# Performance work log

Hardware: AMD Instinct MI355X
Metric: run time of the kernel (lower is better)

The kernel has to match this reference:

```python
import jax, jax.numpy as jnp
import numpy as np

EPS = 1e-8
FS = 10000
WIN_LEN = 256          # N_FRAME
HOP = WIN_LEN // 2     # 128
NFFT = 2 * WIN_LEN     # 512
NUMBAND = 15
MINFREQ = 150
N_INTEL = 30           # N, number of frames per intelligibility segment
BETA = -15.0
DYN_RANGE = 40.0


def _thirdoct(fs, nfft, num_bands, min_freq):
    """One-third octave band matrix (pystoi.utils.thirdoct)."""
    f = np.linspace(0, fs, nfft + 1)[: nfft // 2 + 1]
    k = np.arange(num_bands, dtype=np.float64)
    freq_low = min_freq * np.power(2.0, (2 * k - 1) / 6)
    freq_high = min_freq * np.power(2.0, (2 * k + 1) / 6)
    obm = np.zeros((num_bands, len(f)), dtype=np.float32)
    for i in range(num_bands):
        fl = int(np.argmin(np.square(f - freq_low[i])))
        fh = int(np.argmin(np.square(f - freq_high[i])))
        obm[i, fl:fh] = 1.0
    return obm


def _frame(x, framelen, hop):
    """x: (B, T) -> (B, nf, framelen) sliding frames (static index gather)."""
    T = x.shape[-1]
    nf = (T - framelen) // hop + 1
    idx = np.arange(framelen)[None, :] + hop * np.arange(nf)[:, None]
    return x[:, idx]


def _stoi(est, tgt, win, obm):
    B = tgt.shape[0]
    # ---- VAD: remove silent frames (stable-partition kept frames to front) ----
    xf = _frame(tgt, WIN_LEN, HOP) * win           # (B, nf, L)
    yf = _frame(est, WIN_LEN, HOP) * win
    energies = 20.0 * jnp.log10(jnp.linalg.norm(xf, axis=-1) + EPS)  # (B, nf)
    mask = (energies.max(-1, keepdims=True) - DYN_RANGE - energies) < 0
    nf = xf.shape[1]
    # stable argsort: kept (mask=True -> key 0) frames first, original order preserved
    order = jnp.argsort(jnp.logical_not(mask).astype(jnp.int32), axis=-1)
    xf = jnp.take_along_axis(xf, order[..., None], axis=1)
    yf = jnp.take_along_axis(yf, order[..., None], axis=1)
    counts = mask.sum(-1)                          # (B,) number of kept frames
    keep = (jnp.arange(nf)[None, :] < counts[:, None]).astype(xf.dtype)
    xf = xf * keep[..., None]
    yf = yf * keep[..., None]

    # ---- overlap-and-add (framelen == 2 * hop) -> (B, (nf+1)*HOP) ----
    def ola(fr):
        a = fr[:, :, :HOP].reshape(B, -1)
        b = fr[:, :, HOP:].reshape(B, -1)
        return jnp.pad(a, ((0, 0), (0, HOP))) + jnp.pad(b, ((0, 0), (HOP, 0)))

    x_sil = ola(xf)
    y_sil = ola(yf)

    # mask sorted descending then first element dropped -> ones at positions < count-1
    m = (jnp.arange(nf - 1)[None, :] < (counts[:, None] - 1)).astype(xf.dtype)  # (B, nf-1)

    # ---- STFT via framing + rfft (last frame dropped, as in module) ----
    def stft(x):
        fr = _frame(x, WIN_LEN, HOP)[:, :-1] * win        # (B, nf-1, L)
        return jnp.fft.rfft(fr, n=NFFT, axis=-1)          # (B, nf-1, F)

    x_spec = stft(x_sil) * m[..., None]
    y_spec = stft(y_sil) * m[..., None]

    # ---- one-third octave band energies ----
    x_tob = jnp.sqrt(jnp.einsum('kf,bnf->bkn', obm, jnp.abs(x_spec) ** 2) + EPS)
    y_tob = jnp.sqrt(jnp.einsum('kf,bnf->bkn', obm, jnp.abs(y_spec) ** 2) + EPS)

    # ---- N_INTEL-frame segments (unfold) ----
    n_stft = x_tob.shape[-1]
    M = n_stft - N_INTEL + 1
    sidx = np.arange(N_INTEL)[:, None] + np.arange(M)[None, :]
    x_seg = x_tob[:, :, sidx]                      # (B, K, N, M)
    y_seg = y_tob[:, :, sidx]
    m2 = m[:, N_INTEL - 1:]                        # (B, M)
    x_seg = x_seg * m2[:, None, None, :]
    y_seg = y_seg * m2[:, None, None, :]

    # ---- clipped, normalized correlation (non-extended STOI) ----
    norm_const = jnp.linalg.norm(x_seg, axis=2, keepdims=True) / (
        jnp.linalg.norm(y_seg, axis=2, keepdims=True) + EPS)
    clip_val = 10.0 ** (-BETA / 20.0)
    y_prim = jnp.minimum(y_seg * norm_const, x_seg * (1.0 + clip_val))
    y_prim = y_prim - y_prim.mean(2, keepdims=True)
    x_c = x_seg - x_seg.mean(2, keepdims=True)
    y_prim = y_prim / (jnp.linalg.norm(y_prim, axis=2, keepdims=True) + EPS)
    x_c = x_c / (jnp.linalg.norm(x_c, axis=2, keepdims=True) + EPS)
    corr = (y_prim * x_c).sum(2).mean(1)           # (B, M)
    out = corr.sum(-1) / (m2.sum(-1) + EPS)        # (B,)
    return -out


def setup_inputs() -> dict:
    key = jax.random.key(0)
    k1, k2 = jax.random.split(key)
    B, T = 32, 320000
    targets = jax.random.normal(k1, (B, T), dtype=jnp.float32)
    est_targets = targets + 0.3 * jax.random.normal(k2, (B, T), dtype=jnp.float32)
    win = jnp.asarray(np.hanning(WIN_LEN + 2)[1:-1], dtype=jnp.float32)
    obm = jnp.asarray(_thirdoct(FS, NFFT, NUMBAND, MINFREQ))
    return {"est_targets": est_targets, "targets": targets, "win": win, "obm": obm}


def reference(est_targets, targets, win, obm):
    return _stoi(est_targets, targets, win, obm)
```

## Files before the change

### kernel.cpp

```cpp
#include <hip/hip_runtime.h>
#include <math.h>

#define EPSF 1e-8f
#define WIN_LEN 256
#define HOP 128
#define NBINS 257
#define NUMBAND 15
#define NFRAMES 2499
#define NSTFT 2498
#define N_INTEL 30
#define NSEG 2469
#define NB 32
#define T_LEN 320000
#define CLIP_VAL 5.623413251903491f
#define NHALF 2500
#define AB_STRIDE 2560

typedef float v2f __attribute__((ext_vector_type(2)));
typedef float v4f __attribute__((ext_vector_type(4)));

__device__ __forceinline__ void pk_fma_blo(v2f& d, v2f a, v2f b) {
    asm("v_pk_fma_f32 %0, %1, %2, %0 op_sel:[0,0,0] op_sel_hi:[1,0,1]"
        : "+v"(d) : "v"(a), "v"(b));
}
__device__ __forceinline__ void pk_fma_rot(v2f& d, v2f a, v2f b) {
    asm("v_pk_fma_f32 %0, %1, %2, %0 op_sel:[1,1,0] op_sel_hi:[0,1,1] neg_lo:[1,0,0]"
        : "+v"(d) : "v"(a), "v"(b));
}
__device__ __forceinline__ void pk_rot(v2f& cs, v2f cksk) {
    v2f t;
    asm("v_pk_mul_f32 %0, %1, %2 op_sel:[0,0] op_sel_hi:[1,0]"
        : "=v"(t) : "v"(cs), "v"(cksk));
    asm("v_pk_fma_f32 %0, %0, %1, %2 op_sel:[1,1,0] op_sel_hi:[0,1,1] neg_lo:[1,0,0]"
        : "+v"(cs) : "v"(cksk), "v"(t));
}
__device__ __forceinline__ v2f pk_cmul(v2f a, v2f b) {
    v2f t;
    asm("v_pk_mul_f32 %0, %1, %2 op_sel:[0,0] op_sel_hi:[1,0]"
        : "=v"(t) : "v"(a), "v"(b));
    asm("v_pk_fma_f32 %0, %1, %2, %0 op_sel:[1,1,0] op_sel_hi:[0,1,1] neg_lo:[1,0,0]"
        : "+v"(t) : "v"(a), "v"(b));
    return t;
}

#define WS_COUNTS   0
#define WS_BANDLO   512
#define WS_BANDHI   768
#define WS_ACC      1024
#define WS_SRCFRM   2048
#define WS_XTOB     324096
#define WS_YTOB     5120512

__global__ __launch_bounds__(256)
void k1a_ab(const float* __restrict__ tgt, const float* __restrict__ win,
            float2* __restrict__ ab)
{
    const int b = blockIdx.x;
    const int h = blockIdx.y * 256 + threadIdx.x;
    if (h >= NHALF) return;
    const float* xp = tgt + (size_t)b * T_LEN + (size_t)h * HOP;
    float sa = 0.f, sb = 0.f;
    #pragma unroll 4
    for (int u = 0; u < HOP; u += 4) {
        const float4 xv = *(const float4*)(xp + u);
        const float4 wl = *(const float4*)(win + u);
        const float4 wh = *(const float4*)(win + HOP + u);
        float a;
        a = xv.x * wl.x; sa = fmaf(a, a, sa);
        a = xv.y * wl.y; sa = fmaf(a, a, sa);
        a = xv.z * wl.z; sa = fmaf(a, a, sa);
        a = xv.w * wl.w; sa = fmaf(a, a, sa);
        a = xv.x * wh.x; sb = fmaf(a, a, sb);
        a = xv.y * wh.y; sb = fmaf(a, a, sb);
        a = xv.z * wh.z; sb = fmaf(a, a, sb);
        a = xv.w * wh.w; sb = fmaf(a, a, sb);
    }
    ab[(size_t)b * AB_STRIDE + h] = make_float2(sa, sb);
}

__global__ __launch_bounds__(256)
void k1b_scan(const float2* __restrict__ ab, const float* __restrict__ obm,
              int* __restrict__ counts, int* __restrict__ srcfrm,
              int* __restrict__ band_lo, int* __restrict__ band_hi,
              float* __restrict__ acc)
{
    const int b = blockIdx.x;
    const int tid = threadIdx.x;
    __shared__ float nr[NFRAMES];
    __shared__ float red[256];
    __shared__ int   sc[256];

    const float2* abp = ab + (size_t)b * AB_STRIDE;
    for (int f = tid; f < NFRAMES; f += 256) {
        const float2 p0 = abp[f];
        const float2 p1 = abp[f + 1];
        nr[f] = sqrtf(p0.x + p1.y);
    }
    __syncthreads();

    float mx = 0.f;
    for (int f = tid; f < NFRAMES; f += 256) mx = fmaxf(mx, nr[f]);
    red[tid] = mx;
    __syncthreads();
    for (int s = 128; s > 0; s >>= 1) {
        if (tid < s) red[tid] = fmaxf(red[tid], red[tid + s]);
        __syncthreads();
    }
    const float thr = (red[0] + EPSF) * 0.01f;

    const int c0 = tid * 10;
    const int c1 = (c0 + 10 < NFRAMES) ? c0 + 10 : NFRAMES;
    int lc = 0;
    for (int f = c0; f < c1; ++f) if (nr[f] + EPSF > thr) ++lc;
    sc[tid] = lc;
    __syncthreads();
    #pragma unroll
    for (int off = 1; off < 256; off <<= 1) {
        int u = (tid >= off) ? sc[tid - off] : 0;
        __syncthreads();
        sc[tid] += u;
        __syncthreads();
    }
    if (tid == 0) {
        counts[b] = sc[255];
        acc[b] = 0.f;
    }
    int pos = sc[tid] - lc;
    int* sf = srcfrm + b * NFRAMES;
    for (int f = c0; f < c1; ++f) if (nr[f] + EPSF > thr) sf[pos++] = f;

    if (b == 0 && tid < NUMBAND) {
        int lo = -1, hi = 0;
        for (int k = 0; k < NBINS; ++k) {
            if (obm[tid * NBINS + k] != 0.f) { if (lo < 0) lo = k; hi = k + 1; }
        }
        band_lo[tid] = (lo < 0) ? 0 : lo;
        band_hi[tid] = hi;
    }
    __syncthreads();
    if (b == 0 && tid == 0) {
        int lo = NBINS, hi = 0;
        for (int i = 0; i < NUMBAND; ++i) {
            if (band_lo[i] < lo) lo = band_lo[i];
            if (band_hi[i] > hi) hi = band_hi[i];
        }
        band_lo[NUMBAND] = lo;
        band_hi[NUMBAND] = hi;
    }
}

__global__ __launch_bounds__(64)
void k2_stft_tob(const float* __restrict__ est, const float* __restrict__ tgt,
                 const float* __restrict__ win,
                 const int* __restrict__ counts, const int* __restrict__ srcfrm,
                 const int* __restrict__ band_lo, const int* __restrict__ band_hi,
                 float* __restrict__ xtob, float* __restrict__ ytob)
{
    const int lin = blockIdx.x;
    const int xcd = lin & 7, cidx = lin >> 3;
    const int q = NSTFT >> 3, r = NSTFT & 7;
    const int j = (xcd < r ? xcd * (q + 1) : r * (q + 1) + (xcd - r) * q) + cidx;

    const int b = blockIdx.y;
    const int cntb = counts[b];
    if (j >= cntb - 1) return;

    const int tid = threadIdx.x;
    __shared__ float frf[512];
    __shared__ float sxr[2 * 16 * 68];

    const int* sf = srcfrm + b * NFRAMES;
    const float* xg = tgt + (size_t)b * T_LEN;
    const float* yg = est + (size_t)b * T_LEN;

    {
        const int t4 = 4 * tid;
        const int k0 = sf[j];
        const v4f wa = *(const v4f*)&win[t4];
        v4f xv, yv;
        if (tid < 32) {
            xv = *(const v4f*)&xg[k0 * HOP + t4] * wa;
            yv = *(const v4f*)&yg[k0 * HOP + t4] * wa;
            if (j >= 1) {
                const int km = sf[j - 1];
                const v4f wb = *(const v4f*)&win[HOP + t4];
                xv += *(const v4f*)&xg[km * HOP + HOP + t4] * wb;
                yv += *(const v4f*)&yg[km * HOP + HOP + t4] * wb;
            }
        } else {
            const int kp = sf[j + 1];
            const v4f wb = *(const v4f*)&win[t4 - HOP];
            xv = *(const v4f*)&xg[k0 * HOP + t4] * wa
               + *(const v4f*)&xg[kp * HOP + t4 - HOP] * wb;
            yv = *(const v4f*)&yg[k0 * HOP + t4] * wa
               + *(const v4f*)&yg[kp * HOP + t4 - HOP] * wb;
        }
        xv *= wa; yv *= wa;
        const v4f lo = { xv.x, yv.x, xv.y, yv.y };
        const v4f hi = { xv.z, yv.z, xv.w, yv.w };
        *(v4f*)&frf[2 * t4]     = lo;
        *(v4f*)&frf[2 * t4 + 4] = hi;
    }
    __syncthreads();

    {
        const int m = tid & 3;
        const int c = tid >> 2;
        const float ke = (m == 0) ? 1.f : (m == 2) ? -1.f : 0.f;
        const float ki = (m == 1) ? -1.f : (m == 3) ? 1.f : 0.f;
        const float ang = -0.19634954084936207f * (float)m;
        const float cm0 = __cosf(ang), sm0 = __sinf(ang);
        v2f URe[8], UIm[8];
        float cr = 1.f, sr = 0.f;
        #pragma unroll
        for (int rr = 0; rr < 8; ++rr) {
            const v2f za = *(const v2f*)&frf[2 * (16 * rr + c)];
            const v2f zb = *(const v2f*)&frf[2 * (16 * rr + 128 + c)];
            const v2f pre_re = za + ke * zb;
            const v2f pre_im = ki * zb;
            URe[rr] = cr * pre_re - sr * pre_im;
            UIm[rr] = sr * pre_re + cr * pre_im;
            const float crn = cr * cm0 - sr * sm0;
            sr = sr * cm0 + cr * sm0;
            cr = crn;
        }
        v2f ARe[8], AIm[8];
        {
            const float C2 = 0.70710678118654752f;
            #pragma unroll
            for (int rr = 0; rr < 4; ++rr) {
                ARe[rr] = URe[rr] + URe[rr + 4];
                AIm[rr] = UIm[rr] + UIm[rr + 4];
            }
            v2f dR, dI;
            ARe[4] = URe[0] - URe[4];           AIm[4] = UIm[0] - UIm[4];
            dR = URe[1] - URe[5]; dI = UIm[1] - UIm[5];
            ARe[5] = C2 * (dR + dI);            AIm[5] = C2 * (dI - dR);
            dR = URe[2] - URe[6]; dI = UIm[2] - UIm[6];
            ARe[6] = dI;                        AIm[6] = -dR;
            dR = URe[3] - URe[7]; dI = UIm[3] - UIm[7];
            ARe[7] = C2 * (dI - dR);            AIm[7] = -C2 * (dR + dI);
        }
        v2f BRe[8], BIm[8];
        #pragma unroll
        for (int g = 0; g < 8; g += 4) {
            BRe[g + 0] = ARe[g + 0] + ARe[g + 2];  BIm[g + 0] = AIm[g + 0] + AIm[g + 2];
            BRe[g + 1] = ARe[g + 1] + ARe[g + 3];  BIm[g + 1] = AIm[g + 1] + AIm[g + 3];
            BRe[g + 2] = ARe[g + 0] - ARe[g + 2];  BIm[g + 2] = AIm[g + 0] - AIm[g + 2];
            const v2f dR = ARe[g + 1] - ARe[g + 3], dI = AIm[g + 1] - AIm[g + 3];
            BRe[g + 3] = dI;  BIm[g + 3] = -dR;
        }
        const int kmap[8] = { 0, 4, 2, 6, 1, 5, 3, 7 };
        #pragma unroll
        for (int p = 0; p < 8; ++p) {
            const int pb = p & ~1;
            const float sg = (p & 1) ? -1.f : 1.f;
            const v2f oR = BRe[pb] + sg * BRe[pb + 1];
            const v2f oI = BIm[pb] + sg * BIm[pb + 1];
            const int mj = m + 4 * kmap[p];
            *(v2f*)&sxr[c * 68 + mj * 2]        = (v2f){ oR.x, oI.x };
            *(v2f*)&sxr[1088 + c * 68 + mj * 2] = (v2f){ oR.y, oI.y };
        }
    }
    __syncthreads();

    const int blo = band_lo[NUMBAND];
    const int base = blo & ~31;
    float* px = frf;
    float* py = frf + 224;
    {
        const int m2 = tid & 31;
        const int sig = tid >> 5;
        const float* sbase = sxr + sig * 1088 + m2 * 2;
        const float ang = -0.012271846303085130f * (float)(base + m2);
        const v2f cksk = { __cosf(ang), __sinf(ang) };
        v2f cs = { 1.f, 0.f };
        v2f V[16];
        #pragma unroll
        for (int t0 = 0; t0 < 16; ++t0) {
            const v2f s = *(const v2f*)(sbase + t0 * 68);
            V[t0] = (t0 == 0) ? s : pk_cmul(cs, s);
            pk_rot(cs, cksk);
        }
        v2f G[4][4];
        #pragma unroll
        for (int rr = 0; rr < 4; ++rr) {
            const v2f A = V[rr] + V[rr + 8];
            const v2f B = V[rr] - V[rr + 8];
            const v2f C = V[rr + 4] + V[rr + 12];
            const v2f D = V[rr + 4] - V[rr + 12];
            G[0][rr] = A + C;
            G[2][rr] = A - C;
            G[1][rr] = (v2f){ B.x + D.y, B.y - D.x };
            G[3][rr] = (v2f){ B.x - D.y, B.y + D.x };
        }
        float* pout = sig ? py : px;
        #define C1 0.92387953251f
        #define S1 0.38268343236f
        #define C2c 0.70710678119f
        #define XOUT(P, D, W1R, W1I, W2R, W2I, W3R, W3I) { \
            float xr_ = G[D][0].x, xi_ = G[D][0].y; \
            xr_ += (W1R)*G[D][1].x - (W1I)*G[D][1].y; xi_ += (W1R)*G[D][1].y + (W1I)*G[D][1].x; \
            xr_ += (W2R)*G[D][2].x - (W2I)*G[D][2].y; xi_ += (W2R)*G[D][2].y + (W2I)*G[D][2].x; \
            xr_ += (W3R)*G[D][3].x - (W3I)*G[D][3].y; xi_ += (W3R)*G[D][3].y + (W3I)*G[D][3].x; \
            pout[(P) * 32 + m2] = fmaf(xr_, xr_, xi_ * xi_); }
        XOUT(0, 0,  1.f, 0.f,    1.f, 0.f,    1.f, 0.f)
        XOUT(1, 1,  C1, -S1,     C2c, -C2c,   S1, -C1)
        XOUT(2, 2,  C2c, -C2c,   0.f, -1.f,  -C2c, -C2c)
        XOUT(3, 3,  S1, -C1,    -C2c, -C2c,  -C1,  S1)
        XOUT(4, 0,  0.f, -1.f,  -1.f, 0.f,    0.f,  1.f)
        XOUT(5, 1, -S1, -C1,    -C2c,  C2c,   C1,  S1)
        XOUT(6, 2, -C2c, -C2c,   0.f,  1.f,   C2c, -C2c)
        #undef XOUT
    }
    __syncthreads();

    if (tid < 4 * NUMBAND) {
        const int band = tid >> 2, s = tid & 3;
        const int lop = band_lo[band] - base, hip = band_hi[band] - base;
        const int u0 = lop >> 1, ul = (hip - 1) >> 1;
        float sx = 0.f, sy = 0.f;
        for (int u = u0 + s; u <= ul; u += 4) {
            const v2f pvx = *(const v2f*)&px[2 * u];
            const v2f pvy = *(const v2f*)&py[2 * u];
            const float m0 = (2 * u >= lop) ? 1.f : 0.f;
            const float m1 = (2 * u + 1 < hip) ? 1.f : 0.f;
            sx = fmaf(m0, pvx.x, sx); sx = fmaf(m1, pvx.y, sx);
            sy = fmaf(m0, pvy.x, sy); sy = fmaf(m1, pvy.y, sy);
        }
        sx += __shfl_xor(sx, 1, 64);  sx += __shfl_xor(sx, 2, 64);
        sy += __shfl_xor(sy, 1, 64);  sy += __shfl_xor(sy, 2, 64);
        if (s == 0) {
            xtob[((size_t)b * NUMBAND + band) * NSTFT + j] = sqrtf(sx + EPSF);
            ytob[((size_t)b * NUMBAND + band) * NSTFT + j] = sqrtf(sy + EPSF);
        }
    }
}

__global__ __launch_bounds__(256)
void k3_corr(const float* __restrict__ xtob, const float* __restrict__ ytob,
             const int* __restrict__ counts, float* __restrict__ acc)
{
    const int bb = blockIdx.y;
    const int b = bb / NUMBAND;
    const int band = bb % NUMBAND;
    const int s_base = blockIdx.x * 256;
    const int tid = threadIdx.x;
    const int seg = s_base + tid;

    __shared__ v2f lxy[256 + N_INTEL - 1];
    const float* xr = xtob + ((size_t)b * NUMBAND + band) * NSTFT;
    const float* yr = ytob + ((size_t)b * NUMBAND + band) * NSTFT;
    for (int i = tid; i < 256 + N_INTEL - 1; i += 256) {
        const int g = s_base + i;
        v2f v = { 0.f, 0.f };
        if (g < NSTFT) v = (v2f){ xr[g], yr[g] };
        lxy[i] = v;
    }
    __syncthreads();

    int nvalid = counts[b] - N_INTEL;
    if (nvalid < 0) nvalid = 0;
    if (nvalid > NSEG) nvalid = NSEG;

    float d = 0.f;
    if (seg < nvalid) {
        float xv[N_INTEL], yv[N_INTEL];
        float sx2 = 0.f, sy2 = 0.f;
        #pragma unroll
        for (int i = 0; i < N_INTEL; ++i) {
            const v2f v = lxy[tid + i];
            xv[i] = v.x; yv[i] = v.y;
            sx2 = fmaf(xv[i], xv[i], sx2);
            sy2 = fmaf(yv[i], yv[i], sy2);
        }
        const float nc = sqrtf(sx2) / (sqrtf(sy2) + EPSF);
        float sy = 0.f, sx = 0.f;
        #pragma unroll
        for (int i = 0; i < N_INTEL; ++i) {
            const float yp = fminf(yv[i] * nc, xv[i] * (1.f + CLIP_VAL));
            yv[i] = yp;
            sy += yp; sx += xv[i];
        }
        const float my = sy * (1.f / N_INTEL);
        const float mxm = sx * (1.f / N_INTEL);
        float num = 0.f, dy = 0.f, dx2 = 0.f;
        #pragma unroll
        for (int i = 0; i < N_INTEL; ++i) {
            const float a = yv[i] - my;
            const float c = xv[i] - mxm;
            num = fmaf(a, c, num);
            dy  = fmaf(a, a, dy);
            dx2 = fmaf(c, c, dx2);
        }
        d = num / ((sqrtf(dy) + EPSF) * (sqrtf(dx2) + EPSF));
    }

    #pragma unroll
    for (int o = 32; o > 0; o >>= 1) d += __shfl_down(d, o, 64);
    __shared__ float wsum[4];
    const int lane = threadIdx.x & 63, wid = threadIdx.x >> 6;
    if (lane == 0) wsum[wid] = d;
    __syncthreads();
    if (threadIdx.x == 0) {
        atomicAdd(&acc[b], wsum[0] + wsum[1] + wsum[2] + wsum[3]);
    }
}

__global__ void k4_final(const float* __restrict__ acc, const int* __restrict__ counts,
                         float* __restrict__ out)
{
    const int b = threadIdx.x;
    if (b < NB) {
        int nvalid = counts[b] - N_INTEL;
        if (nvalid < 0) nvalid = 0;
        if (nvalid > NSEG) nvalid = NSEG;
        out[b] = -(acc[b] * (1.f / NUMBAND)) / ((float)nvalid + EPSF);
    }
}

extern "C" void kernel_launch(void* const* d_in, const int* in_sizes, int n_in,
                              void* d_out, int out_size, void* d_ws, size_t ws_size,
                              hipStream_t stream) {
    (void)in_sizes; (void)n_in; (void)out_size; (void)ws_size;
    const float* est = (const float*)d_in[0];
    const float* tgt = (const float*)d_in[1];
    const float* win = (const float*)d_in[2];
    const float* obm = (const float*)d_in[3];
    float* out = (float*)d_out;

    char* ws = (char*)d_ws;
    int*   counts  = (int*)(ws + WS_COUNTS);
    int*   band_lo = (int*)(ws + WS_BANDLO);
    int*   band_hi = (int*)(ws + WS_BANDHI);
    float* acc     = (float*)(ws + WS_ACC);
    int*   srcfrm  = (int*)(ws + WS_SRCFRM);
    float* xtob    = (float*)(ws + WS_XTOB);
    float* ytob    = (float*)(ws + WS_YTOB);
    float2* ab     = (float2*)xtob;

    k1a_ab<<<dim3(NB, 10), dim3(256), 0, stream>>>(tgt, win, ab);
    k1b_scan<<<dim3(NB), dim3(256), 0, stream>>>(ab, obm, counts, srcfrm,
                                                 band_lo, band_hi, acc);
    k2_stft_tob<<<dim3(NSTFT, NB), dim3(64), 0, stream>>>(est, tgt, win, counts, srcfrm,
                                                          band_lo, band_hi, xtob, ytob);
    k3_corr<<<dim3((NSEG + 255) / 256, NB * NUMBAND), dim3(256), 0, stream>>>(xtob, ytob,
                                                                              counts, acc);
    k4_final<<<1, NB, 0, stream>>>(acc, counts, out);
}
```

Baseline: 191.0 us.

## Precompute FFT twiddle tables, use packed-FP32 butterflies, fold final kernel into corr

Twiddle factors for both FFT stages are computed once in the first kernel and stored in workspace tables. The STFT kernel loads them instead of running sin/cos and rotation recurrences per block. The radix butterflies are rewritten with explicit v_pk_add/mul/fma inline asm, and the trivial DFT outputs are special-cased. The k4 finalisation kernel is removed: k3 scales its partial sum and atomically adds straight into the output, which k1a zeroes. This saves one launch and some ALU work, at the cost of extra global loads for the twiddles and more inline-asm complexity.

```diff
diff --git a/kernel.cpp b/kernel.cpp
--- a/kernel.cpp
+++ b/kernel.cpp
@@ -27,12 +27,54 @@
     asm("v_pk_fma_f32 %0, %1, %2, %0 op_sel:[1,1,0] op_sel_hi:[0,1,1] neg_lo:[1,0,0]"
         : "+v"(d) : "v"(a), "v"(b));
 }
-__device__ __forceinline__ void pk_rot(v2f& cs, v2f cksk) {
-    v2f t;
+__device__ __forceinline__ void pk_fma_nbhi(v2f& d, v2f a, v2f b) {
+    asm("v_pk_fma_f32 %0, %1, %2, %0 op_sel:[0,1,0] op_sel_hi:[1,1,1] neg_lo:[1,0,0] neg_hi:[1,0,0]"
+        : "+v"(d) : "v"(a), "v"(b));
+}
+__device__ __forceinline__ void pk_fma_s(v2f& d, v2f a, float s) {
+    const v2f bv = { s, s };
+    asm("v_pk_fma_f32 %0, %1, %2, %0"
+        : "+v"(d) : "v"(a), "v"(bv));
+}
+__device__ __forceinline__ v2f pk_mul_blo(v2f a, v2f b) {
+    v2f d;
     asm("v_pk_mul_f32 %0, %1, %2 op_sel:[0,0] op_sel_hi:[1,0]"
-        : "=v"(t) : "v"(cs), "v"(cksk));
-    asm("v_pk_fma_f32 %0, %0, %1, %2 op_sel:[1,1,0] op_sel_hi:[0,1,1] neg_lo:[1,0,0]"
-        : "+v"(cs) : "v"(cksk), "v"(t));
+        : "=v"(d) : "v"(a), "v"(b));
+    return d;
+}
+__device__ __forceinline__ v2f pk_mul_bhi(v2f a, v2f b) {
+    v2f d;
+    asm("v_pk_mul_f32 %0, %1, %2 op_sel:[0,1] op_sel_hi:[1,1]"
+        : "=v"(d) : "v"(a), "v"(b));
+    return d;
+}
+__device__ __forceinline__ v2f pk_mul_s(v2f a, float s) {
+    const v2f bv = { s, s };
+    v2f d;
+    asm("v_pk_mul_f32 %0, %1, %2" : "=v"(d) : "v"(a), "v"(bv));
+    return d;
+}
+__device__ __forceinline__ v2f pk_add(v2f a, v2f b) {
+    v2f d;
+    asm("v_pk_add_f32 %0, %1, %2" : "=v"(d) : "v"(a), "v"(b));
+    return d;
+}
+__device__ __forceinline__ v2f pk_sub(v2f a, v2f b) {
+    v2f d;
+    asm("v_pk_add_f32 %0, %1, %2 neg_lo:[0,1] neg_hi:[0,1]" : "=v"(d) : "v"(a), "v"(b));
+    return d;
+}
+__device__ __forceinline__ v2f pk_bmi(v2f B, v2f D) {
+    v2f d;
+    asm("v_pk_add_f32 %0, %1, %2 op_sel:[1,0] op_sel_hi:[0,1] neg_hi:[1,0]"
+        : "=v"(d) : "v"(D), "v"(B));
+    return d;
+}
+__device__ __forceinline__ v2f pk_bpi(v2f B, v2f D) {
+    v2f d;
+    asm("v_pk_add_f32 %0, %1, %2 op_sel:[1,0] op_sel_hi:[0,1] neg_lo:[1,0]"
+        : "=v"(d) : "v"(D), "v"(B));
+    return d;
 }
 __device__ __forceinline__ v2f pk_cmul(v2f a, v2f b) {
     v2f t;
@@ -42,47 +84,92 @@
         : "+v"(t) : "v"(a), "v"(b));
     return t;
 }
+__device__ __forceinline__ void pk_cfma(v2f& acc, v2f g, float wr, float wi) {
+    const v2f wv = { wr, wi };
+    pk_fma_blo(acc, g, wv);
+    pk_fma_rot(acc, g, wv);
+}
 
 #define WS_COUNTS   0
 #define WS_BANDLO   512
 #define WS_BANDHI   768
-#define WS_ACC      1024
-#define WS_SRCFRM   2048
-#define WS_XTOB     324096
-#define WS_YTOB     5120512
+#define WS_TW1      1024
+#define WS_TW2      1536
+#define WS_SRCFRM   5632
+#define WS_XTOB     325632
+#define WS_YTOB     5121792
 
 __global__ __launch_bounds__(256)
 void k1a_ab(const float* __restrict__ tgt, const float* __restrict__ win,
-            float2* __restrict__ ab)
+            const float* __restrict__ obm, float2* __restrict__ ab,
+            int* __restrict__ band_lo, int* __restrict__ band_hi,
+            v2f* __restrict__ tw1, v2f* __restrict__ tw2,
+            float* __restrict__ out_)
 {
     const int b = blockIdx.x;
-    const int h = blockIdx.y * 256 + threadIdx.x;
-    if (h >= NHALF) return;
-    const float* xp = tgt + (size_t)b * T_LEN + (size_t)h * HOP;
-    float sa = 0.f, sb = 0.f;
-    #pragma unroll 4
-    for (int u = 0; u < HOP; u += 4) {
-        const float4 xv = *(const float4*)(xp + u);
-        const float4 wl = *(const float4*)(win + u);
-        const float4 wh = *(const float4*)(win + HOP + u);
-        float a;
-        a = xv.x * wl.x; sa = fmaf(a, a, sa);
-        a = xv.y * wl.y; sa = fmaf(a, a, sa);
-        a = xv.z * wl.z; sa = fmaf(a, a, sa);
-        a = xv.w * wl.w; sa = fmaf(a, a, sa);
-        a = xv.x * wh.x; sb = fmaf(a, a, sb);
-        a = xv.y * wh.y; sb = fmaf(a, a, sb);
-        a = xv.z * wh.z; sb = fmaf(a, a, sb);
-        a = xv.w * wh.w; sb = fmaf(a, a, sb);
-    }
-    ab[(size_t)b * AB_STRIDE + h] = make_float2(sa, sb);
+    const int tid = threadIdx.x;
+    const int h = blockIdx.y * 256 + tid;
+    if (h < NHALF) {
+        const float* xp = tgt + (size_t)b * T_LEN + (size_t)h * HOP;
+        float sa = 0.f, sb = 0.f;
+        #pragma unroll 4
+        for (int u = 0; u < HOP; u += 4) {
+            const float4 xv = *(const float4*)(xp + u);
+            const float4 wl = *(const float4*)(win + u);
+            const float4 wh = *(const float4*)(win + HOP + u);
+            float a;
+            a = xv.x * wl.x; sa = fmaf(a, a, sa);
+            a = xv.y * wl.y; sa = fmaf(a, a, sa);
+            a = xv.z * wl.z; sa = fmaf(a, a, sa);
+            a = xv.w * wl.w; sa = fmaf(a, a, sa);
+            a = xv.x * wh.x; sb = fmaf(a, a, sb);
+            a = xv.y * wh.y; sb = fmaf(a, a, sb);
+            a = xv.z * wh.z; sb = fmaf(a, a, sb);
+            a = xv.w * wh.w; sb = fmaf(a, a, sb);
+        }
+        ab[(size_t)b * AB_STRIDE + h] = make_float2(sa, sb);
+    }
+
+    if (b == 0 && blockIdx.y == 0) {
+        __shared__ int sbase;
+        if (tid < NUMBAND) {
+            int lo = -1, hi = 0;
+            for (int k = 0; k < NBINS; ++k) {
+                if (obm[tid * NBINS + k] != 0.f) { if (lo < 0) lo = k; hi = k + 1; }
+            }
+            band_lo[tid] = (lo < 0) ? 0 : lo;
+            band_hi[tid] = hi;
+        }
+        __syncthreads();
+        if (tid == 0) {
+            int lo = NBINS, hi = 0;
+            for (int i = 0; i < NUMBAND; ++i) {
+                if (band_lo[i] < lo) lo = band_lo[i];
+                if (band_hi[i] > hi) hi = band_hi[i];
+            }
+            band_lo[NUMBAND] = lo;
+            band_hi[NUMBAND] = hi;
+            sbase = lo & ~31;
+        }
+        __syncthreads();
+        const int base = sbase;
+        if (tid < NB) out_[tid] = 0.f;
+        if (tid < 32) {
+            const int m = tid >> 3, rr = tid & 7;
+            const float ang = -0.19634954084936207f * (float)(m * rr);
+            tw1[tid] = (v2f){ cosf(ang), sinf(ang) };
+        }
+        for (int i = tid; i < 512; i += 256) {
+            const int m2 = i >> 4, t0 = i & 15;
+            const float ang = -0.012271846303085130f * (float)((base + m2) * t0);
+            tw2[i] = (v2f){ cosf(ang), sinf(ang) };
+        }
+    }
 }
 
 __global__ __launch_bounds__(256)
-void k1b_scan(const float2* __restrict__ ab, const float* __restrict__ obm,
-              int* __restrict__ counts, int* __restrict__ srcfrm,
-              int* __restrict__ band_lo, int* __restrict__ band_hi,
-              float* __restrict__ acc)
+void k1b_scan(const float2* __restrict__ ab,
+              int* __restrict__ counts, int* __restrict__ srcfrm)
 {
     const int b = blockIdx.x;
     const int tid = threadIdx.x;
@@ -121,32 +208,10 @@
         sc[tid] += u;
         __syncthreads();
     }
-    if (tid == 0) {
-        counts[b] = sc[255];
-        acc[b] = 0.f;
-    }
+    if (tid == 0) counts[b] = sc[255];
     int pos = sc[tid] - lc;
     int* sf = srcfrm + b * NFRAMES;
     for (int f = c0; f < c1; ++f) if (nr[f] + EPSF > thr) sf[pos++] = f;
-
-    if (b == 0 && tid < NUMBAND) {
-        int lo = -1, hi = 0;
-        for (int k = 0; k < NBINS; ++k) {
-            if (obm[tid * NBINS + k] != 0.f) { if (lo < 0) lo = k; hi = k + 1; }
-        }
-        band_lo[tid] = (lo < 0) ? 0 : lo;
-        band_hi[tid] = hi;
-    }
-    __syncthreads();
-    if (b == 0 && tid == 0) {
-        int lo = NBINS, hi = 0;
-        for (int i = 0; i < NUMBAND; ++i) {
-            if (band_lo[i] < lo) lo = band_lo[i];
-            if (band_hi[i] > hi) hi = band_hi[i];
-        }
-        band_lo[NUMBAND] = lo;
-        band_hi[NUMBAND] = hi;
-    }
 }
 
 __global__ __launch_bounds__(64)
@@ -154,6 +219,7 @@
                  const float* __restrict__ win,
                  const int* __restrict__ counts, const int* __restrict__ srcfrm,
                  const int* __restrict__ band_lo, const int* __restrict__ band_hi,
+                 const v2f* __restrict__ tw1, const v2f* __restrict__ tw2,
                  float* __restrict__ xtob, float* __restrict__ ytob)
 {
     const int lin = blockIdx.x;
@@ -206,57 +272,62 @@
     {
         const int m = tid & 3;
         const int c = tid >> 2;
+        v4f t1r[4];
+        {
+            const v4f* p = (const v4f*)(tw1 + m * 8);
+            #pragma unroll
+            for (int i = 0; i < 4; ++i) t1r[i] = p[i];
+        }
         const float ke = (m == 0) ? 1.f : (m == 2) ? -1.f : 0.f;
         const float ki = (m == 1) ? -1.f : (m == 3) ? 1.f : 0.f;
-        const float ang = -0.19634954084936207f * (float)m;
-        const float cm0 = __cosf(ang), sm0 = __sinf(ang);
         v2f URe[8], UIm[8];
-        float cr = 1.f, sr = 0.f;
         #pragma unroll
         for (int rr = 0; rr < 8; ++rr) {
             const v2f za = *(const v2f*)&frf[2 * (16 * rr + c)];
             const v2f zb = *(const v2f*)&frf[2 * (16 * rr + 128 + c)];
-            const v2f pre_re = za + ke * zb;
-            const v2f pre_im = ki * zb;
-            URe[rr] = cr * pre_re - sr * pre_im;
-            UIm[rr] = sr * pre_re + cr * pre_im;
-            const float crn = cr * cm0 - sr * sm0;
-            sr = sr * cm0 + cr * sm0;
-            cr = crn;
+            v2f pre_re = za; pk_fma_s(pre_re, zb, ke);
+            const v2f pre_im = pk_mul_s(zb, ki);
+            const v2f tw = (rr & 1) ? t1r[rr >> 1].zw : t1r[rr >> 1].xy;
+            v2f ur = pk_mul_blo(pre_re, tw); pk_fma_nbhi(ur, pre_im, tw);
+            v2f ui = pk_mul_bhi(pre_re, tw); pk_fma_blo(ui, pre_im, tw);
+            URe[rr] = ur; UIm[rr] = ui;
         }
         v2f ARe[8], AIm[8];
         {
             const float C2 = 0.70710678118654752f;
+            v2f dR, dI;
             #pragma unroll
             for (int rr = 0; rr < 4; ++rr) {
-                ARe[rr] = URe[rr] + URe[rr + 4];
-                AIm[rr] = UIm[rr] + UIm[rr + 4];
+                ARe[rr] = pk_add(URe[rr], URe[rr + 4]);
+                AIm[rr] = pk_add(UIm[rr], UIm[rr + 4]);
             }
-            v2f dR, dI;
-            ARe[4] = URe[0] - URe[4];           AIm[4] = UIm[0] - UIm[4];
-            dR = URe[1] - URe[5]; dI = UIm[1] - UIm[5];
-            ARe[5] = C2 * (dR + dI);            AIm[5] = C2 * (dI - dR);
-            dR = URe[2] - URe[6]; dI = UIm[2] - UIm[6];
-            ARe[6] = dI;                        AIm[6] = -dR;
-            dR = URe[3] - URe[7]; dI = UIm[3] - UIm[7];
-            ARe[7] = C2 * (dI - dR);            AIm[7] = -C2 * (dR + dI);
+            ARe[4] = pk_sub(URe[0], URe[4]);     AIm[4] = pk_sub(UIm[0], UIm[4]);
+            dR = pk_sub(URe[1], URe[5]); dI = pk_sub(UIm[1], UIm[5]);
+            ARe[5] = pk_mul_s(pk_add(dR, dI), C2);
+            AIm[5] = pk_mul_s(pk_sub(dI, dR), C2);
+            dR = pk_sub(URe[2], URe[6]); dI = pk_sub(UIm[2], UIm[6]);
+            ARe[6] = dI;                         AIm[6] = pk_mul_s(dR, -1.f);
+            dR = pk_sub(URe[3], URe[7]); dI = pk_sub(UIm[3], UIm[7]);
+            ARe[7] = pk_mul_s(pk_sub(dI, dR), C2);
+            AIm[7] = pk_mul_s(pk_add(dR, dI), -C2);
         }
         v2f BRe[8], BIm[8];
         #pragma unroll
         for (int g = 0; g < 8; g += 4) {
-            BRe[g + 0] = ARe[g + 0] + ARe[g + 2];  BIm[g + 0] = AIm[g + 0] + AIm[g + 2];
-            BRe[g + 1] = ARe[g + 1] + ARe[g + 3];  BIm[g + 1] = AIm[g + 1] + AIm[g + 3];
-            BRe[g + 2] = ARe[g + 0] - ARe[g + 2];  BIm[g + 2] = AIm[g + 0] - AIm[g + 2];
-            const v2f dR = ARe[g + 1] - ARe[g + 3], dI = AIm[g + 1] - AIm[g + 3];
-            BRe[g + 3] = dI;  BIm[g + 3] = -dR;
+            BRe[g + 0] = pk_add(ARe[g + 0], ARe[g + 2]);  BIm[g + 0] = pk_add(AIm[g + 0], AIm[g + 2]);
+            BRe[g + 1] = pk_add(ARe[g + 1], ARe[g + 3]);  BIm[g + 1] = pk_add(AIm[g + 1], AIm[g + 3]);
+            BRe[g + 2] = pk_sub(ARe[g + 0], ARe[g + 2]);  BIm[g + 2] = pk_sub(AIm[g + 0], AIm[g + 2]);
+            const v2f dR = pk_sub(ARe[g + 1], ARe[g + 3]);
+            const v2f dI = pk_sub(AIm[g + 1], AIm[g + 3]);
+            BRe[g + 3] = dI;  BIm[g + 3] = pk_mul_s(dR, -1.f);
         }
         const int kmap[8] = { 0, 4, 2, 6, 1, 5, 3, 7 };
         #pragma unroll
         for (int p = 0; p < 8; ++p) {
             const int pb = p & ~1;
-            const float sg = (p & 1) ? -1.f : 1.f;
-            const v2f oR = BRe[pb] + sg * BRe[pb + 1];
-            const v2f oI = BIm[pb] + sg * BIm[pb + 1];
+            v2f oR, oI;
+            if (p & 1) { oR = pk_sub(BRe[pb], BRe[pb + 1]); oI = pk_sub(BIm[pb], BIm[pb + 1]); }
+            else       { oR = pk_add(BRe[pb], BRe[pb + 1]); oI = pk_add(BIm[pb], BIm[pb + 1]); }
             const int mj = m + 4 * kmap[p];
             *(v2f*)&sxr[c * 68 + mj * 2]        = (v2f){ oR.x, oI.x };
             *(v2f*)&sxr[1088 + c * 68 + mj * 2] = (v2f){ oR.y, oI.y };
@@ -272,43 +343,54 @@
         const int m2 = tid & 31;
         const int sig = tid >> 5;
         const float* sbase = sxr + sig * 1088 + m2 * 2;
-        const float ang = -0.012271846303085130f * (float)(base + m2);
-        const v2f cksk = { __cosf(ang), __sinf(ang) };
-        v2f cs = { 1.f, 0.f };
+        v4f t2r[8];
+        {
+            const v4f* p = (const v4f*)(tw2 + m2 * 16);
+            #pragma unroll
+            for (int i = 0; i < 8; ++i) t2r[i] = p[i];
+        }
         v2f V[16];
         #pragma unroll
         for (int t0 = 0; t0 < 16; ++t0) {
             const v2f s = *(const v2f*)(sbase + t0 * 68);
-            V[t0] = (t0 == 0) ? s : pk_cmul(cs, s);
-            pk_rot(cs, cksk);
+            const v2f tw = (t0 & 1) ? t2r[t0 >> 1].zw : t2r[t0 >> 1].xy;
+            V[t0] = pk_cmul(tw, s);
         }
         v2f G[4][4];
         #pragma unroll
         for (int rr = 0; rr < 4; ++rr) {
-            const v2f A = V[rr] + V[rr + 8];
-            const v2f B = V[rr] - V[rr + 8];
-            const v2f C = V[rr + 4] + V[rr + 12];
-            const v2f D = V[rr + 4] - V[rr + 12];
-            G[0][rr] = A + C;
-            G[2][rr] = A - C;
-            G[1][rr] = (v2f){ B.x + D.y, B.y - D.x };
-            G[3][rr] = (v2f){ B.x - D.y, B.y + D.x };
+            const v2f A = pk_add(V[rr], V[rr + 8]);
+            const v2f B = pk_sub(V[rr], V[rr + 8]);
+            const v2f C = pk_add(V[rr + 4], V[rr + 12]);
+            const v2f D = pk_sub(V[rr + 4], V[rr + 12]);
+            G[0][rr] = pk_add(A, C);
+            G[2][rr] = pk_sub(A, C);
+            G[1][rr] = pk_bmi(B, D);
+            G[3][rr] = pk_bpi(B, D);
         }
         float* pout = sig ? py : px;
         #define C1 0.92387953251f
         #define S1 0.38268343236f
         #define C2c 0.70710678119f
+        {
+            const v2f a_ = pk_add(pk_add(G[0][0], G[0][1]), pk_add(G[0][2], G[0][3]));
+            pout[0 * 32 + m2] = fmaf(a_.x, a_.x, a_.y * a_.y);
+        }
         #define XOUT(P, D, W1R, W1I, W2R, W2I, W3R, W3I) { \
-            float xr_ = G[D][0].x, xi_ = G[D][0].y; \
-            xr_ += (W1R)*G[D][1].x - (W1I)*G[D][1].y; xi_ += (W1R)*G[D][1].y + (W1I)*G[D][1].x; \
-            xr_ += (W2R)*G[D][2].x - (W2I)*G[D][2].y; xi_ += (W2R)*G[D][2].y + (W2I)*G[D][2].x; \
-            xr_ += (W3R)*G[D][3].x - (W3I)*G[D][3].y; xi_ += (W3R)*G[D][3].y + (W3I)*G[D][3].x; \
-            pout[(P) * 32 + m2] = fmaf(xr_, xr_, xi_ * xi_); }
-        XOUT(0, 0,  1.f, 0.f,    1.f, 0.f,    1.f, 0.f)
+            v2f a_ = G[D][0]; \
+            pk_cfma(a_, G[D][1], W1R, W1I); \
+            pk_cfma(a_, G[D][2], W2R, W2I); \
+            pk_cfma(a_, G[D][3], W3R, W3I); \
+            pout[(P) * 32 + m2] = fmaf(a_.x, a_.x, a_.y * a_.y); }
         XOUT(1, 1,  C1, -S1,     C2c, -C2c,   S1, -C1)
         XOUT(2, 2,  C2c, -C2c,   0.f, -1.f,  -C2c, -C2c)
         XOUT(3, 3,  S1, -C1,    -C2c, -C2c,  -C1,  S1)
-        XOUT(4, 0,  0.f, -1.f,  -1.f, 0.f,    0.f,  1.f)
+        {
+            const v2f t1_ = pk_sub(G[0][0], G[0][2]);
+            const v2f t2_ = pk_sub(G[0][1], G[0][3]);
+            const v2f a_ = pk_bmi(t1_, t2_);
+            pout[4 * 32 + m2] = fmaf(a_.x, a_.x, a_.y * a_.y);
+        }
         XOUT(5, 1, -S1, -C1,    -C2c,  C2c,   C1,  S1)
         XOUT(6, 2, -C2c, -C2c,   0.f,  1.f,   C2c, -C2c)
         #undef XOUT
@@ -339,7 +421,7 @@
 
 __global__ __launch_bounds__(256)
 void k3_corr(const float* __restrict__ xtob, const float* __restrict__ ytob,
-             const int* __restrict__ counts, float* __restrict__ acc)
+             const int* __restrict__ counts, float* __restrict__ out_)
 {
     const int bb = blockIdx.y;
     const int b = bb / NUMBAND;
@@ -403,19 +485,8 @@
     if (lane == 0) wsum[wid] = d;
     __syncthreads();
     if (threadIdx.x == 0) {
-        atomicAdd(&acc[b], wsum[0] + wsum[1] + wsum[2] + wsum[3]);
-    }
-}
-
-__global__ void k4_final(const float* __restrict__ acc, const int* __restrict__ counts,
-                         float* __restrict__ out)
-{
-    const int b = threadIdx.x;
-    if (b < NB) {
-        int nvalid = counts[b] - N_INTEL;
-        if (nvalid < 0) nvalid = 0;
-        if (nvalid > NSEG) nvalid = NSEG;
-        out[b] = -(acc[b] * (1.f / NUMBAND)) / ((float)nvalid + EPSF);
+        const float scale = -1.f / ((float)NUMBAND * ((float)nvalid + EPSF));
+        atomicAdd(&out_[b], (wsum[0] + wsum[1] + wsum[2] + wsum[3]) * scale);
     }
 }
 
@@ -433,18 +504,19 @@
     int*   counts  = (int*)(ws + WS_COUNTS);
     int*   band_lo = (int*)(ws + WS_BANDLO);
     int*   band_hi = (int*)(ws + WS_BANDHI);
-    float* acc     = (float*)(ws + WS_ACC);
+    v2f*   tw1     = (v2f*)(ws + WS_TW1);
+    v2f*   tw2     = (v2f*)(ws + WS_TW2);
     int*   srcfrm  = (int*)(ws + WS_SRCFRM);
     float* xtob    = (float*)(ws + WS_XTOB);
     float* ytob    = (float*)(ws + WS_YTOB);
     float2* ab     = (float2*)xtob;
 
-    k1a_ab<<<dim3(NB, 10), dim3(256), 0, stream>>>(tgt, win, ab);
-    k1b_scan<<<dim3(NB), dim3(256), 0, stream>>>(ab, obm, counts, srcfrm,
-                                                 band_lo, band_hi, acc);
+    k1a_ab<<<dim3(NB, 10), dim3(256), 0, stream>>>(tgt, win, obm, ab,
+                                                   band_lo, band_hi, tw1, tw2, out);
+    k1b_scan<<<dim3(NB), dim3(256), 0, stream>>>(ab, counts, srcfrm);
     k2_stft_tob<<<dim3(NSTFT, NB), dim3(64), 0, stream>>>(est, tgt, win, counts, srcfrm,
-                                                          band_lo, band_hi, xtob, ytob);
+                                                          band_lo, band_hi, tw1, tw2,
+                                                          xtob, ytob);
     k3_corr<<<dim3((NSEG + 255) / 256, NB * NUMBAND), dim3(256), 0, stream>>>(xtob, ytob,
-                                                                              counts, acc);
-    k4_final<<<1, NB, 0, stream>>>(acc, counts, out);
-}
+                                                                              counts, out);
+}
```

After: 223.4 us. +17.0%, slower.
